# Kernel tuning notes

Hardware: AMD Instinct MI355X
Metric: run time of the kernel (lower is better)

Reference implementation:

```python
import jax, jax.numpy as jnp
import numpy as np

K = 10
NUM_BLKS = 6
LN_EPS = 1e-6
NODE_D = 64


def layer_norm(x, g, b):
    m = jnp.mean(x, axis=-1, keepdims=True)
    v = jnp.var(x, axis=-1, keepdims=True)
    return (x - m) * jax.lax.rsqrt(v + LN_EPS) * g + b


def setup_inputs() -> dict:
    key = jax.random.key(0)
    B, N_c, N_t, D_S, D_F = 4, 4096, 1024, 3, 4
    D_IN = 4 + D_S + D_F  # obs-embed(4) + s + f
    ks = jax.random.split(key, 32)
    sc = 0.02
    inp = {
        "s_ctx": jax.random.normal(ks[0], (B, N_c, D_S), jnp.float32),
        "f_ctx": jax.random.normal(ks[1], (B, N_c, D_F), jnp.float32),
        "s_test": jax.random.normal(ks[2], (B, N_t, D_S), jnp.float32),
        "valid_lens_ctx": jax.random.randint(ks[3], (B,), N_c // 2, N_c + 1).astype(jnp.int32),
        # embed_obs: nn.Embed(2, 4)
        "emb_obs": jax.random.normal(ks[4], (2, 4), jnp.float32) * sc,
        # embed_all: MLP([256,128,64], gelu)
        "ea_W0": jax.random.normal(ks[5], (D_IN, 256), jnp.float32) * sc, "ea_b0": jnp.zeros((256,), jnp.float32),
        "ea_W1": jax.random.normal(ks[6], (256, 128), jnp.float32) * sc, "ea_b1": jnp.zeros((128,), jnp.float32),
        "ea_W2": jax.random.normal(ks[7], (128, NODE_D), jnp.float32) * sc, "ea_b2": jnp.zeros((NODE_D,), jnp.float32),
        # top-level LayerNorm
        "ln_g": jnp.ones((NODE_D,), jnp.float32), "ln_b": jnp.zeros((NODE_D,), jnp.float32),
        # GraphKRBlock params, stacked over NUM_BLKS blocks
        "blk_Wm0": jax.random.normal(ks[8], (NUM_BLKS, NODE_D + 1, 128), jnp.float32) * sc,
        "blk_bm0": jnp.zeros((NUM_BLKS, 128), jnp.float32),
        "blk_Wm1": jax.random.normal(ks[9], (NUM_BLKS, 128, NODE_D), jnp.float32) * sc,
        "blk_bm1": jnp.zeros((NUM_BLKS, NODE_D), jnp.float32),
        "blk_Wu0": jax.random.normal(ks[10], (NUM_BLKS, 2 * NODE_D, 128), jnp.float32) * sc,
        "blk_bu0": jnp.zeros((NUM_BLKS, 128), jnp.float32),
        "blk_Wu1": jax.random.normal(ks[11], (NUM_BLKS, 128, NODE_D), jnp.float32) * sc,
        "blk_bu1": jnp.zeros((NUM_BLKS, NODE_D), jnp.float32),
        "blk_lng": jnp.ones((NUM_BLKS, NODE_D), jnp.float32),
        "blk_lnb": jnp.zeros((NUM_BLKS, NODE_D), jnp.float32),
        # head: MLP([256,64,2], gelu)
        "hd_W0": jax.random.normal(ks[12], (NODE_D, 256), jnp.float32) * sc, "hd_b0": jnp.zeros((256,), jnp.float32),
        "hd_W1": jax.random.normal(ks[13], (256, 64), jnp.float32) * sc, "hd_b1": jnp.zeros((64,), jnp.float32),
        "hd_W2": jax.random.normal(ks[14], (64, 2), jnp.float32) * sc, "hd_b2": jnp.zeros((2,), jnp.float32),
    }
    return inp


def reference(s_ctx, f_ctx, s_test, valid_lens_ctx,
              emb_obs, ea_W0, ea_b0, ea_W1, ea_b1, ea_W2, ea_b2, ln_g, ln_b,
              blk_Wm0, blk_bm0, blk_Wm1, blk_bm1, blk_Wu0, blk_bu0, blk_Wu1, blk_bu1,
              blk_lng, blk_lnb, hd_W0, hd_b0, hd_W1, hd_b1, hd_W2, hd_b2):
    B, N_c, _ = s_ctx.shape
    N_t = s_test.shape[1]

    # --- per-sample O(n^2) KNN graph build (custom_k_nearest_senders, l2 dist) ---
    mask = jnp.arange(N_c)[None, :] < valid_lens_ctx[:, None]          # [B,N_c]
    s_send = jnp.where(mask[..., None], s_ctx, 1e6)                    # invalid -> far away
    rx = jnp.concatenate([s_ctx, s_test], axis=1)                      # [B,N,d_s] receivers
    d = jnp.sqrt(jnp.sum((rx[:, :, None, :] - s_send[:, None, :, :]) ** 2, axis=-1))  # [B,N,N_c]
    negd, senders = jax.lax.top_k(-d, K)                               # k-nearest: [B,N,K]
    dists = -negd                                                       # ascending distances

    # --- embeddings: stack(embed_obs, s, f) -> embed_all MLP -> LayerNorm ---
    def embed(x):
        h = jax.nn.gelu(x @ ea_W0 + ea_b0)
        h = jax.nn.gelu(h @ ea_W1 + ea_b1)
        h = h @ ea_W2 + ea_b2
        return layer_norm(h, ln_g, ln_b)

    ctx_in = jnp.concatenate(
        [jnp.broadcast_to(emb_obs[1], (B, N_c, emb_obs.shape[1])), s_ctx, f_ctx], axis=-1)
    test_in = jnp.concatenate(
        [jnp.broadcast_to(emb_obs[0], (B, N_t, emb_obs.shape[1])), s_test,
         jnp.zeros((B, N_t, f_ctx.shape[-1]), f_ctx.dtype)], axis=-1)
    nodes = jnp.concatenate([embed(ctx_in), embed(test_in)], axis=1)   # [B,N,64]

    # --- num_blks GraphKRBlock message-passing blocks ---
    bidx = jnp.arange(B)[:, None, None]
    w = jax.nn.softmax(-dists, axis=-1)                                # kernel weights per receiver
    for i in range(NUM_BLKS):
        sf = nodes[bidx, senders]                                      # gather senders [B,N,K,64]
        m_in = jnp.concatenate([sf, dists[..., None]], axis=-1)        # [B,N,K,65]
        m = jax.nn.gelu(m_in @ blk_Wm0[i] + blk_bm0[i]) @ blk_Wm1[i] + blk_bm1[i]
        agg = jnp.einsum('bnk,bnkd->bnd', w, m)                        # scatter-to-receivers
        u_in = jnp.concatenate([nodes, agg], axis=-1)                  # [B,N,128]
        upd = jax.nn.gelu(u_in @ blk_Wu0[i] + blk_bu0[i]) @ blk_Wu1[i] + blk_bu1[i]
        nodes = layer_norm(nodes + upd, blk_lng[i], blk_lnb[i])

    # --- head on test nodes ---
    x_t = nodes[:, N_c:, :]                                            # [B,N_t,64]
    h = jax.nn.gelu(x_t @ hd_W0 + hd_b0)
    h = jax.nn.gelu(h @ hd_W1 + hd_b1)
    f_dist = h @ hd_W2 + hd_b2                                         # [B,N_t,2]
    f_mu, f_log_var = jnp.split(f_dist, 2, axis=-1)
    f_std = jnp.exp(f_log_var / 2)                                     # min_std = 0.0
    return f_mu, f_std
```

## Files before the change

kernel.cpp:

```cpp
#include <hip/hip_runtime.h>
#include <math.h>

#define BB 4
#define NC 4096
#define NT 1024
#define NN (NC + NT)
#define NODES (BB * NN)
#define DD 64
#define KNN 10
#define NBLK 6
#define BIGF 3.0e38f
#define LM 5

typedef __attribute__((ext_vector_type(8))) short short8;
typedef __attribute__((ext_vector_type(4))) float f32x4;
typedef __attribute__((ext_vector_type(4))) int int4v;

__device__ __forceinline__ unsigned short f2bf(float f) {
    unsigned int u = __float_as_uint(f);
    unsigned int r = (u + 0x7fffu + ((u >> 16) & 1u)) >> 16;
    return (unsigned short)r;
}
__device__ __forceinline__ float bf2f(unsigned short h) {
    return __uint_as_float(((unsigned int)h) << 16);
}

__device__ __forceinline__ float gelu_f(float x) {
    const float c0 = 0.7978845608028654f;
    float x3 = x * x * x;
    float z2 = 2.0f * c0 * (x + 0.044715f * x3);
    float e = __expf(z2);
    float r = __builtin_amdgcn_rcpf(1.0f + e);
    return x - x * r;
}

__device__ __forceinline__ float wave_sum(float v) {
#pragma unroll
    for (int off = 32; off > 0; off >>= 1) v += __shfl_xor(v, off, 64);
    return v;
}

__device__ __forceinline__ f32x4 mfma_bf16(short8 a, short8 b, f32x4 c) {
    asm("v_mfma_f32_16x16x32_bf16 %0, %1, %2, %0" : "+v"(c) : "v"(a), "v"(b));
    return c;
}


__global__ __launch_bounds__(256) void k_convw(
    const float* __restrict__ Wm0, const float* __restrict__ Wm1,
    const float* __restrict__ Wu0, const float* __restrict__ Wu1,
    const float* __restrict__ bm0,
    const float* __restrict__ eW0, const float* __restrict__ eW1,
    const float* __restrict__ eW2,
    const float* __restrict__ hW0, const float* __restrict__ hW1,
    const float* __restrict__ sctx, const int* __restrict__ valid_lens,
    unsigned short* __restrict__ wtm0, unsigned short* __restrict__ wtm1p,
    unsigned short* __restrict__ wtu0, unsigned short* __restrict__ wtu1,
    float* __restrict__ wdp, float* __restrict__ bm0p,
    unsigned short* __restrict__ wte0, unsigned short* __restrict__ wte1,
    unsigned short* __restrict__ wte2,
    unsigned short* __restrict__ wth0, unsigned short* __restrict__ wth1,
    float4* __restrict__ s4)
{
    int t = blockIdx.x * 256 + threadIdx.x;
    if (t < 49152) {
        int i = t / 8192, r = t % 8192, n = r / 64, k = r % 64;
        wtm0[t] = f2bf(Wm0[(i * 65 + k) * 128 + n]);
    } else if (t < 98304) {
        int u = t - 49152;
        int i = u / 8192, r = u % 8192, n = r / 128, cp = r % 128;
        int col = ((cp & 7) << 4) | (cp >> 3);
        wtm1p[u] = f2bf(Wm1[(i * 128 + col) * 64 + n]);
    } else if (t < 196608) {
        int u = t - 98304;
        int i = u / 16384, r = u % 16384, n = r / 128, k = r % 128;
        wtu0[u] = f2bf(Wu0[(i * 128 + k) * 128 + n]);
    } else if (t < 245760) {
        int u = t - 196608;
        int i = u / 8192, r = u % 8192, n = r / 128, k = r % 128;
        wtu1[u] = f2bf(Wu1[(i * 128 + k) * 64 + n]);
    } else if (t < 246528) {
        int u = t - 245760;
        int i = u / 128, cp = u % 128;
        int col = ((cp & 7) << 4) | (cp >> 3);
        wdp[u] = Wm0[(i * 65 + 64) * 128 + col];
    } else if (t < 247296) {
        int u = t - 246528;
        int i = u / 128, cp = u % 128;
        int col = ((cp & 7) << 4) | (cp >> 3);
        bm0p[u] = bm0[i * 128 + col];
    } else if (t < 255488) {
        int u = t - 247296;
        int n = u / 32, k = u % 32;
        wte0[u] = (k < 11) ? f2bf(eW0[k * 256 + n]) : 0;
    } else if (t < 288256) {
        int u = t - 255488;
        int n = u / 256, k = u % 256;
        wte1[u] = f2bf(eW1[k * 128 + n]);
    } else if (t < 296448) {
        int u = t - 288256;
        int n = u / 128, k = u % 128;
        wte2[u] = f2bf(eW2[k * 64 + n]);
    } else if (t < 312832) {
        int u = t - 296448;
        int n = u / 64, k = u % 64;
        wth0[u] = f2bf(hW0[k * 256 + n]);
    } else if (t < 329216) {
        int u = t - 312832;
        int n = u / 256, k = u % 256;
        wth1[u] = f2bf(hW1[k * 64 + n]);
    } else if (t < 329216 + BB * NC) {
        int u = t - 329216;
        int b = u / NC, j = u % NC;
        bool ok = j < valid_lens[b];
        float x = ok ? sctx[u * 3] : 1.0e6f;
        float y = ok ? sctx[u * 3 + 1] : 1.0e6f;
        float z = ok ? sctx[u * 3 + 2] : 1.0e6f;
        s4[u] = make_float4(x, y, z, 0.0f);
    }
}

__global__ __launch_bounds__(256) void k_embed2(
    const float* __restrict__ s_ctx, const float* __restrict__ f_ctx,
    const float* __restrict__ s_test, const float* __restrict__ emb_obs,
    const unsigned short* __restrict__ WT0, const float* __restrict__ b0,
    const unsigned short* __restrict__ WT1, const float* __restrict__ b1,
    const unsigned short* __restrict__ WT2, const float* __restrict__ b2,
    const float* __restrict__ g, const float* __restrict__ bta,
    const unsigned short* __restrict__ Wm0n,
    unsigned short* __restrict__ nodes,
    unsigned short* __restrict__ Pout)
{
    __shared__ unsigned short H0[4][16 * 256];
    __shared__ unsigned short H1[4][16 * 128];
    __shared__ unsigned short XO[4][16 * 64];
    int t = threadIdx.x;
    int wave = t >> 6, lane = t & 63, lr = lane & 15, lk = lane >> 4;
    int rb = wave * 16;
    int n0 = blockIdx.x * 64;
    int bq = n0 / NN, nloc0 = n0 % NN;
    bool is_ctx = nloc0 < NC;
    int nr = nloc0 + rb + lr;
    float xv[8];
#pragma unroll
    for (int j = 0; j < 8; ++j) xv[j] = 0.0f;
    if (lk == 0) {
        const float* eb = emb_obs + (is_ctx ? 4 : 0);
        xv[0] = eb[0]; xv[1] = eb[1]; xv[2] = eb[2]; xv[3] = eb[3];
        if (is_ctx) {
            const float* sp = s_ctx + ((size_t)(bq * NC + nr)) * 3;
            const float* fp = f_ctx + ((size_t)(bq * NC + nr)) * 4;
            xv[4] = sp[0]; xv[5] = sp[1]; xv[6] = sp[2]; xv[7] = fp[0];
        } else {
            const float* sp = s_test + ((size_t)(bq * NT + nr - NC)) * 3;
            xv[4] = sp[0]; xv[5] = sp[1]; xv[6] = sp[2];
        }
    } else if (lk == 1 && is_ctx) {
        const float* fp = f_ctx + ((size_t)(bq * NC + nr)) * 4;
        xv[0] = fp[1]; xv[1] = fp[2]; xv[2] = fp[3];
    }
    short8 a;
#pragma unroll
    for (int j = 0; j < 8; ++j) a[j] = (short)f2bf(xv[j]);

    f32x4 acc0[16];
#pragma unroll
    for (int nt = 0; nt < 16; ++nt) {
        short8 bb = *(const short8*)(WT0 + (nt * 16 + lr) * 32 + lk * 8);
        f32x4 z = (f32x4){0.f, 0.f, 0.f, 0.f};
        acc0[nt] = mfma_bf16(a, bb, z);
    }
    unsigned short* h0 = &H0[wave][0];
#pragma unroll
    for (int nt = 0; nt < 16; ++nt) {
        int col = nt * 16 + lr;
        float bias = b0[col];
        int u = col >> 3;
#pragma unroll
        for (int j = 0; j < 4; ++j) {
            int row = lk * 4 + j;
            float v = gelu_f(acc0[nt][j] + bias);
            int us = (u & 16) | ((u ^ row) & 15);
            h0[row * 256 + us * 8 + (col & 7)] = f2bf(v);
        }
    }
    f32x4 acc1[8];
#pragma unroll
    for (int nt = 0; nt < 8; ++nt) acc1[nt] = (f32x4){0.f, 0.f, 0.f, 0.f};
#pragma unroll
    for (int ks = 0; ks < 8; ++ks) {
        int u = ks * 4 + lk;
        int us = (u & 16) | ((u ^ lr) & 15);
        short8 aa = *(const short8*)(&h0[lr * 256 + us * 8]);
#pragma unroll
        for (int nt = 0; nt < 8; ++nt) {
            short8 bb = *(const short8*)(WT1 + (nt * 16 + lr) * 256 + ks * 32 + lk * 8);
            acc1[nt] = mfma_bf16(aa, bb, acc1[nt]);
        }
    }
    unsigned short* h1 = &H1[wave][0];
#pragma unroll
    for (int nt = 0; nt < 8; ++nt) {
        int col = nt * 16 + lr;
        float bias = b1[col];
        int u = col >> 3;
#pragma unroll
        for (int j = 0; j < 4; ++j) {
            int row = lk * 4 + j;
            float v = gelu_f(acc1[nt][j] + bias);
            int us = (u ^ row) & 15;
            h1[row * 128 + us * 8 + (col & 7)] = f2bf(v);
        }
    }
    f32x4 acc2[4];
#pragma unroll
    for (int nt = 0; nt < 4; ++nt) acc2[nt] = (f32x4){0.f, 0.f, 0.f, 0.f};
#pragma unroll
    for (int ks = 0; ks < 4; ++ks) {
        int u = ks * 4 + lk;
        int us = (u ^ lr) & 15;
        short8 aa = *(const short8*)(&h1[lr * 128 + us * 8]);
#pragma unroll
        for (int nt = 0; nt < 4; ++nt) {
            short8 bb = *(const short8*)(WT2 + (nt * 16 + lr) * 128 + ks * 32 + lk * 8);
            acc2[nt] = mfma_bf16(aa, bb, acc2[nt]);
        }
    }
    float vals[4][4];
#pragma unroll
    for (int j = 0; j < 4; ++j)
#pragma unroll
        for (int nt = 0; nt < 4; ++nt)
            vals[j][nt] = acc2[nt][j] + b2[nt * 16 + lr];
    unsigned short* xo = &XO[wave][0];
#pragma unroll
    for (int j = 0; j < 4; ++j) {
        float s = vals[j][0] + vals[j][1] + vals[j][2] + vals[j][3];
#pragma unroll
        for (int m = 1; m < 16; m <<= 1) s += __shfl_xor(s, m, 64);
        float mean = s * (1.0f / 64.0f);
        float vs = 0.0f;
#pragma unroll
        for (int nt = 0; nt < 4; ++nt) { float d = vals[j][nt] - mean; vs += d * d; }
#pragma unroll
        for (int m = 1; m < 16; m <<= 1) vs += __shfl_xor(vs, m, 64);
        float inv = rsqrtf(vs * (1.0f / 64.0f) + 1e-6f);
        int row = lk * 4 + j;
        int node = n0 + rb + row;
#pragma unroll
        for (int nt = 0; nt < 4; ++nt) {
            int col = nt * 16 + lr;
            float o = (vals[j][nt] - mean) * inv * g[col] + bta[col];
            unsigned short ob = f2bf(o);
            nodes[(size_t)node * 64 + col] = ob;
            xo[row * 64 + ((col >> 3) ^ (row & 7)) * 8 + (col & 7)] = ob;
        }
    }
    f32x4 accP[8];
#pragma unroll
    for (int nt = 0; nt < 8; ++nt) accP[nt] = (f32x4){0.f, 0.f, 0.f, 0.f};
#pragma unroll
    for (int ks = 0; ks < 2; ++ks) {
        short8 aa = *(const short8*)(&xo[lr * 64 + ((ks * 4 + lk) ^ (lr & 7)) * 8]);
#pragma unroll
        for (int nt = 0; nt < 8; ++nt) {
            short8 bb = *(const short8*)(Wm0n + (nt * 16 + lr) * 64 + ks * 32 + lk * 8);
            accP[nt] = mfma_bf16(aa, bb, accP[nt]);
        }
    }
#pragma unroll
    for (int j = 0; j < 4; ++j) {
        int node = n0 + rb + lk * 4 + j;
        short8 ps;
#pragma unroll
        for (int nt = 0; nt < 8; ++nt) ps[nt] = (short)f2bf(accP[nt][j]);
        *(short8*)(Pout + (size_t)node * 128 + lr * 8) = ps;
    }
}

__global__ __launch_bounds__(256) void k_topk(
    const float4* __restrict__ s4, const float* __restrict__ s_ctx,
    const float* __restrict__ s_test,
    float* __restrict__ dists, int* __restrict__ senders, float* __restrict__ wout)
{
    __shared__ float cd[4 * 64 * 11];
    __shared__ float slotv[4][4][16];
    __shared__ int   sloti[4][4][16];
    __shared__ int   cnt[4][4];
    int wave = threadIdx.x >> 6;
    int lane = threadIdx.x & 63;
    int r0 = blockIdx.x * 16 + wave * 4;
    int b = r0 / NN;
    const float4* sc = s4 + (size_t)b * NC;
    float px[4], py[4], pz[4];
#pragma unroll
    for (int q = 0; q < 4; ++q) {
        int n = (r0 + q) % NN;
        const float* p = (n < NC) ? &s_ctx[(size_t)(b * NC + n) * 3]
                                  : &s_test[(size_t)(b * NT + (n - NC)) * 3];
        px[q] = p[0]; py[q] = p[1]; pz[q] = p[2];
    }
    float bq[4][LM];
#pragma unroll
    for (int q = 0; q < 4; ++q)
#pragma unroll
        for (int k = 0; k < LM; ++k) bq[q][k] = BIGF;
#pragma unroll 8
    for (int i = 0; i < 64; ++i) {
        int j = lane + (i << 6);
        float4 s = sc[j];
#pragma unroll
        for (int q = 0; q < 4; ++q) {
            float dx = px[q] - s.x, dy = py[q] - s.y, dz = pz[q] - s.z;
            float d2 = fmaf(dx, dx, fmaf(dy, dy, dz * dz));
#pragma unroll
            for (int k = LM - 1; k >= 1; --k)
                bq[q][k] = __builtin_amdgcn_fmed3f(bq[q][k - 1], bq[q][k], d2);
            bq[q][0] = fminf(bq[q][0], d2);
        }
    }
    int base = (wave * 64 + lane) * 11;
    float T[4];
#pragma unroll
    for (int q = 0; q < 4; ++q) {
#pragma unroll
        for (int k = 0; k < LM; ++k) cd[base + k] = bq[q][k];
        cd[base + LM] = BIGF;
        __builtin_amdgcn_wave_barrier();
        int head = 0;
        float Tl = BIGF;
#pragma unroll
        for (int rr = 0; rr < KNN; ++rr) {
            float v = cd[base + head];
            float mv = v;
#pragma unroll
            for (int off = 32; off > 0; off >>= 1) mv = fminf(mv, __shfl_xor(mv, off, 64));
            unsigned long long ball = __ballot(v == mv);
            int win = __ffsll(ball) - 1;
            if (lane == win) head++;
            Tl = mv;
        }
        T[q] = Tl;
    }
    if (lane < 4) cnt[wave][lane] = 0;
    __builtin_amdgcn_wave_barrier();
#pragma unroll 4
    for (int i = 0; i < 64; ++i) {
        int j = lane + (i << 6);
        float4 s = sc[j];
#pragma unroll
        for (int q = 0; q < 4; ++q) {
            float dx = px[q] - s.x, dy = py[q] - s.y, dz = pz[q] - s.z;
            float v = fmaf(dx, dx, fmaf(dy, dy, dz * dz));
            if (v <= T[q]) {
                int slot = atomicAdd(&cnt[wave][q], 1);
                if (slot < 16) { slotv[wave][q][slot] = v; sloti[wave][q][slot] = j; }
            }
        }
    }
    __builtin_amdgcn_wave_barrier();
#pragma unroll
    for (int q = 0; q < 4; ++q) {
        int count = cnt[wave][q];
        if (count > 16) count = 16;
        float e = 0.0f, d = 0.0f;
        int isel = 0, rank = 0;
        bool own = lane < count;
        if (own) {
            float myv = slotv[wave][q][lane];
            int myi = sloti[wave][q][lane];
            for (int j = 0; j < count; ++j) {
                float vj = slotv[wave][q][j];
                int ij = sloti[wave][q][j];
                rank += (vj < myv || (vj == myv && ij < myi)) ? 1 : 0;
            }
            own = rank < KNN;
            if (own) {
                isel = myi;
                d = sqrtf(myv);
                e = __expf(-d);
            }
        }
        float ssum = wave_sum(e);
        if (own) {
            size_t o = (size_t)(r0 + q) * KNN + rank;
            dists[o] = d;
            senders[o] = isel;
            wout[o] = e / ssum;
        }
    }
}

__global__ __launch_bounds__(256) void k_blk(
    const unsigned short* __restrict__ nodes_in,
    const unsigned short* __restrict__ P,
    const float* __restrict__ dists, const int* __restrict__ senders,
    const float* __restrict__ w,
    const float* __restrict__ wdp, const float* __restrict__ bm0p,
    const unsigned short* __restrict__ Wm1p,
    const float* __restrict__ bm1,
    const unsigned short* __restrict__ WTu0,
    const float* __restrict__ bu0,
    const unsigned short* __restrict__ WTu1,
    const float* __restrict__ bu1,
    const float* __restrict__ lng, const float* __restrict__ lnb,
    const unsigned short* __restrict__ Wm0n,
    const int doP,
    unsigned short* __restrict__ nodes_out,
    unsigned short* __restrict__ Pout,
    const int doHead, const int testOnly,
    const unsigned short* __restrict__ wth0,
    const float* __restrict__ hb0,
    const unsigned short* __restrict__ wth1,
    const float* __restrict__ hb1,
    const float* __restrict__ hW2, const float* __restrict__ hb2,
    float* __restrict__ out)
{
    __shared__ unsigned short X[16 * 64];
    __shared__ unsigned short G[16 * 128];
    __shared__ unsigned short AG[16 * 64];
    __shared__ unsigned short H[16 * 128];
    __shared__ unsigned short XO[16 * 64];
    __shared__ unsigned short HH[16 * 256];
    __shared__ unsigned short HH1[16 * 72];
    __shared__ int   sidE[160];
    __shared__ float dE[160], wE[160];
    int l = threadIdx.x;
    int wave = l >> 6, lane = l & 63;
    int bid = blockIdx.x;
    int tile = testOnly ? ((bid >> 6) * 320 + 256 + (bid & 63))
                        : ((bid & 7) * 160 + (bid >> 3));
    int n0 = tile * 16;
    int b = n0 / NN;
    size_t bbase = (size_t)b * NN;
    int e0 = n0 * KNN;
    if (l < 160) {
        sidE[l] = senders[e0 + l];
        dE[l]   = dists[e0 + l];
        wE[l]   = w[e0 + l];
    }
    if (l < 128) {
        int row = l >> 3, u = l & 7;
        int4v v = *(const int4v*)(nodes_in + ((size_t)(n0 + row)) * 64 + u * 8);
        *(int4v*)(&X[row * 64 + (u ^ (row & 7)) * 8]) = v;
    }
    __syncthreads();
    float wd0 = wdp[2 * lane], wd1 = wdp[2 * lane + 1];
    float bb0 = bm0p[2 * lane], bb1 = bm0p[2 * lane + 1];
    const unsigned int* Pb = (const unsigned int*)P;
    unsigned int* G32 = (unsigned int*)G;
#pragma unroll
    for (int nn = 0; nn < 4; ++nn) {
        int n = wave * 4 + nn;
        float a0 = 0.0f, a1 = 0.0f;
#pragma unroll
        for (int k = 0; k < KNN; ++k) {
            int e = n * KNN + k;
            int sid = sidE[e];
            float dd = dE[e], ww = wE[e];
            unsigned int pr = Pb[(bbase + sid) * 64 + lane];
            float p0 = __uint_as_float(pr << 16);
            float p1 = __uint_as_float(pr & 0xFFFF0000u);
            float g0 = gelu_f(fmaf(dd, wd0, p0 + bb0));
            float g1 = gelu_f(fmaf(dd, wd1, p1 + bb1));
            a0 = fmaf(ww, g0, a0);
            a1 = fmaf(ww, g1, a1);
        }
        unsigned int pk = (unsigned int)f2bf(a0) | ((unsigned int)f2bf(a1) << 16);
        G32[n * 64 + ((lane >> 2) ^ n) * 4 + (lane & 3)] = pk;
    }
    __syncthreads();
    if (wave != 0) return;
    int lr = lane & 15, lk = lane >> 4;
    f32x4 accA[4];
#pragma unroll
    for (int nt = 0; nt < 4; ++nt) accA[nt] = (f32x4){0.f, 0.f, 0.f, 0.f};
#pragma unroll
    for (int ks = 0; ks < 4; ++ks) {
        short8 a = *(const short8*)(&G[lr * 128 + ((ks * 4 + lk) ^ lr) * 8]);
#pragma unroll
        for (int nt = 0; nt < 4; ++nt) {
            short8 bb = *(const short8*)(Wm1p + (nt * 16 + lr) * 128 + ks * 32 + lk * 8);
            accA[nt] = mfma_bf16(a, bb, accA[nt]);
        }
    }
#pragma unroll
    for (int nt = 0; nt < 4; ++nt) {
        int col = nt * 16 + lr;
        float bias = bm1[col];
#pragma unroll
        for (int j = 0; j < 4; ++j) {
            int row = lk * 4 + j;
            AG[row * 64 + ((col >> 3) ^ (row & 7)) * 8 + (col & 7)] =
                f2bf(accA[nt][j] + bias);
        }
    }
    f32x4 acc[8];
#pragma unroll
    for (int nt = 0; nt < 8; ++nt) acc[nt] = (f32x4){0.f, 0.f, 0.f, 0.f};
#pragma unroll
    for (int ks = 0; ks < 4; ++ks) {
        short8 a;
        if (ks < 2) a = *(const short8*)(&X[lr * 64 + ((ks * 4 + lk) ^ (lr & 7)) * 8]);
        else        a = *(const short8*)(&AG[lr * 64 + (((ks - 2) * 4 + lk) ^ (lr & 7)) * 8]);
#pragma unroll
        for (int nt = 0; nt < 8; ++nt) {
            short8 bb = *(const short8*)(WTu0 + (nt * 16 + lr) * 128 + ks * 32 + lk * 8);
            acc[nt] = mfma_bf16(a, bb, acc[nt]);
        }
    }
#pragma unroll
    for (int nt = 0; nt < 8; ++nt) {
        int col = nt * 16 + lr;
        float bias = bu0[col];
#pragma unroll
        for (int j = 0; j < 4; ++j) {
            int lrow = lk * 4 + j;
            float v = gelu_f(acc[nt][j] + bias);
            H[lrow * 128 + ((col >> 3) ^ lrow) * 8 + (col & 7)] = f2bf(v);
        }
    }
    f32x4 acc2[4];
#pragma unroll
    for (int nt = 0; nt < 4; ++nt) acc2[nt] = (f32x4){0.f, 0.f, 0.f, 0.f};
#pragma unroll
    for (int ks = 0; ks < 4; ++ks) {
        short8 a = *(const short8*)(&H[lr * 128 + ((ks * 4 + lk) ^ lr) * 8]);
#pragma unroll
        for (int nt = 0; nt < 4; ++nt) {
            short8 bb = *(const short8*)(WTu1 + (nt * 16 + lr) * 128 + ks * 32 + lk * 8);
            acc2[nt] = mfma_bf16(a, bb, acc2[nt]);
        }
    }
    float vals[4][4];
#pragma unroll
    for (int j = 0; j < 4; ++j) {
        int row = lk * 4 + j;
#pragma unroll
        for (int nt = 0; nt < 4; ++nt) {
            int col = nt * 16 + lr;
            float x = bf2f(X[row * 64 + ((col >> 3) ^ (row & 7)) * 8 + (col & 7)]);
            vals[j][nt] = x + acc2[nt][j] + bu1[col];
        }
    }
#pragma unroll
    for (int j = 0; j < 4; ++j) {
        int row = lk * 4 + j;
        float s = vals[j][0] + vals[j][1] + vals[j][2] + vals[j][3];
#pragma unroll
        for (int mm = 1; mm < 16; mm <<= 1) s += __shfl_xor(s, mm, 64);
        float mean = s * (1.0f / 64.0f);
        float vs = 0.0f;
#pragma unroll
        for (int nt = 0; nt < 4; ++nt) { float d = vals[j][nt] - mean; vs += d * d; }
#pragma unroll
        for (int mm = 1; mm < 16; mm <<= 1) vs += __shfl_xor(vs, mm, 64);
        float inv = rsqrtf(vs * (1.0f / 64.0f) + 1e-6f);
#pragma unroll
        for (int nt = 0; nt < 4; ++nt) {
            int col = nt * 16 + lr;
            float o = (vals[j][nt] - mean) * inv * lng[col] + lnb[col];
            unsigned short ob = f2bf(o);
            nodes_out[((size_t)(n0 + row)) * 64 + col] = ob;
            XO[row * 64 + ((col >> 3) ^ (row & 7)) * 8 + (col & 7)] = ob;
        }
    }
    if (doP) {
        f32x4 accP[8];
#pragma unroll
        for (int nt = 0; nt < 8; ++nt) accP[nt] = (f32x4){0.f, 0.f, 0.f, 0.f};
#pragma unroll
        for (int ks = 0; ks < 2; ++ks) {
            short8 aa = *(const short8*)(&XO[lr * 64 + ((ks * 4 + lk) ^ (lr & 7)) * 8]);
#pragma unroll
            for (int nt = 0; nt < 8; ++nt) {
                short8 bb = *(const short8*)(Wm0n + (nt * 16 + lr) * 64 + ks * 32 + lk * 8);
                accP[nt] = mfma_bf16(aa, bb, accP[nt]);
            }
        }
#pragma unroll
        for (int j = 0; j < 4; ++j) {
            int node = n0 + lk * 4 + j;
            short8 ps;
#pragma unroll
            for (int nt = 0; nt < 8; ++nt) ps[nt] = (short)f2bf(accP[nt][j]);
            *(short8*)(Pout + (size_t)node * 128 + lr * 8) = ps;
        }
    }
    if (doHead) {
        int nloc = n0 % NN;
        int bq = n0 / NN;
#pragma unroll
        for (int half = 0; half < 2; ++half) {
            f32x4 ah[8];
#pragma unroll
            for (int nt = 0; nt < 8; ++nt) ah[nt] = (f32x4){0.f, 0.f, 0.f, 0.f};
#pragma unroll
            for (int ks = 0; ks < 2; ++ks) {
                short8 aa = *(const short8*)(&XO[lr * 64 + ((ks * 4 + lk) ^ (lr & 7)) * 8]);
#pragma unroll
                for (int nt = 0; nt < 8; ++nt) {
                    int col16 = half * 8 + nt;
                    short8 bb = *(const short8*)(wth0 + (col16 * 16 + lr) * 64 + ks * 32 + lk * 8);
                    ah[nt] = mfma_bf16(aa, bb, ah[nt]);
                }
            }
#pragma unroll
            for (int nt = 0; nt < 8; ++nt) {
                int col = (half * 8 + nt) * 16 + lr;
                float bias = hb0[col];
                int u = col >> 3;
#pragma unroll
                for (int j = 0; j < 4; ++j) {
                    int row = lk * 4 + j;
                    float v = gelu_f(ah[nt][j] + bias);
                    int us = (u & 16) | ((u ^ row) & 15);
                    HH[row * 256 + us * 8 + (col & 7)] = f2bf(v);
                }
            }
        }
        f32x4 a1h[4];
#pragma unroll
        for (int nt = 0; nt < 4; ++nt) a1h[nt] = (f32x4){0.f, 0.f, 0.f, 0.f};
#pragma unroll
        for (int ks = 0; ks < 8; ++ks) {
            int u = ks * 4 + lk;
            int us = (u & 16) | ((u ^ lr) & 15);
            short8 aa = *(const short8*)(&HH[lr * 256 + us * 8]);
#pragma unroll
            for (int nt = 0; nt < 4; ++nt) {
                short8 bb = *(const short8*)(wth1 + (nt * 16 + lr) * 256 + ks * 32 + lk * 8);
                a1h[nt] = mfma_bf16(aa, bb, a1h[nt]);
            }
        }
#pragma unroll
        for (int nt = 0; nt < 4; ++nt) {
            int col = nt * 16 + lr;
            float bias = hb1[col];
#pragma unroll
            for (int j = 0; j < 4; ++j) {
                int row = lk * 4 + j;
                HH1[row * 72 + col] = f2bf(gelu_f(a1h[nt][j] + bias));
            }
        }
        int task = lane >> 1;
        int row = task >> 1;
        int o = task & 1;
        int t2 = lane & 1;
        float pp = 0.0f;
#pragma unroll
        for (int d = 0; d < 32; ++d) {
            int dd = t2 * 32 + d;
            pp += bf2f(HH1[row * 72 + dd]) * hW2[dd * 2 + o];
        }
        pp += __shfl_xor(pp, 1, 64);
        if (t2 == 0) {
            int gg = bq * NT + (nloc - NC) + row;
            if (o == 0) out[gg] = pp + hb2[0];
            else        out[BB * NT + gg] = __expf(0.5f * (pp + hb2[1]));
        }
    }
}

extern "C" void kernel_launch(void* const* d_in, const int* in_sizes, int n_in,
                              void* d_out, int out_size, void* d_ws, size_t ws_size,
                              hipStream_t stream)
{
    (void)in_sizes; (void)n_in; (void)out_size; (void)ws_size;
    const float* s_ctx   = (const float*)d_in[0];
    const float* f_ctx   = (const float*)d_in[1];
    const float* s_test  = (const float*)d_in[2];
    const int*   valid   = (const int*)d_in[3];
    const float* emb_obs = (const float*)d_in[4];
    const float* ea_W0   = (const float*)d_in[5];
    const float* ea_b0   = (const float*)d_in[6];
    const float* ea_W1   = (const float*)d_in[7];
    const float* ea_b1   = (const float*)d_in[8];
    const float* ea_W2   = (const float*)d_in[9];
    const float* ea_b2   = (const float*)d_in[10];
    const float* ln_g    = (const float*)d_in[11];
    const float* ln_b    = (const float*)d_in[12];
    const float* blk_Wm0 = (const float*)d_in[13];
    const float* blk_bm0 = (const float*)d_in[14];
    const float* blk_Wm1 = (const float*)d_in[15];
    const float* blk_bm1 = (const float*)d_in[16];
    const float* blk_Wu0 = (const float*)d_in[17];
    const float* blk_bu0 = (const float*)d_in[18];
    const float* blk_Wu1 = (const float*)d_in[19];
    const float* blk_bu1 = (const float*)d_in[20];
    const float* blk_lng = (const float*)d_in[21];
    const float* blk_lnb = (const float*)d_in[22];
    const float* hd_W0   = (const float*)d_in[23];
    const float* hd_b0   = (const float*)d_in[24];
    const float* hd_W1   = (const float*)d_in[25];
    const float* hd_b1   = (const float*)d_in[26];
    const float* hd_W2   = (const float*)d_in[27];
    const float* hd_b2   = (const float*)d_in[28];

    char* p = (char*)d_ws;
    auto alloc = [&](size_t bytes) { char* r = p; p += (bytes + 255) & ~(size_t)255; return r; };
    unsigned short* nodesA = (unsigned short*)alloc((size_t)NODES * 64 * 2);
    unsigned short* nodesB = (unsigned short*)alloc((size_t)NODES * 64 * 2);
    unsigned short* PA     = (unsigned short*)alloc((size_t)NODES * 128 * 2);
    unsigned short* PB     = (unsigned short*)alloc((size_t)NODES * 128 * 2);
    float* dists   = (float*)alloc((size_t)NODES * KNN * 4);
    float* wbuf    = (float*)alloc((size_t)NODES * KNN * 4);
    int*   senders = (int*)alloc((size_t)NODES * KNN * 4);
    unsigned short* wtm0  = (unsigned short*)alloc((size_t)6 * 8192 * 2);
    unsigned short* wtm1p = (unsigned short*)alloc((size_t)6 * 8192 * 2);
    unsigned short* wtu0  = (unsigned short*)alloc((size_t)6 * 16384 * 2);
    unsigned short* wtu1  = (unsigned short*)alloc((size_t)6 * 8192 * 2);
    float* wdp  = (float*)alloc((size_t)6 * 128 * 4);
    float* bm0p = (float*)alloc((size_t)6 * 128 * 4);
    unsigned short* wte0 = (unsigned short*)alloc((size_t)8192 * 2);
    unsigned short* wte1 = (unsigned short*)alloc((size_t)32768 * 2);
    unsigned short* wte2 = (unsigned short*)alloc((size_t)8192 * 2);
    unsigned short* wth0 = (unsigned short*)alloc((size_t)16384 * 2);
    unsigned short* wth1 = (unsigned short*)alloc((size_t)16384 * 2);
    float4* s4 = (float4*)alloc((size_t)BB * NC * 16);

    k_convw<<<1350, 256, 0, stream>>>(
        blk_Wm0, blk_Wm1, blk_Wu0, blk_Wu1, blk_bm0,
        ea_W0, ea_W1, ea_W2, hd_W0, hd_W1, s_ctx, valid,
        wtm0, wtm1p, wtu0, wtu1, wdp, bm0p, wte0, wte1, wte2, wth0, wth1, s4);

    k_embed2<<<NODES / 64, 256, 0, stream>>>(s_ctx, f_ctx, s_test, emb_obs,
        wte0, ea_b0, wte1, ea_b1, wte2, ea_b2, ln_g, ln_b, wtm0, nodesA, PA);

    k_topk<<<NODES / 16, 256, 0, stream>>>(s4, s_ctx, s_test,
                                           dists, senders, wbuf);

    unsigned short* nin = nodesA; unsigned short* nout = nodesB;
    unsigned short* pin = PA;     unsigned short* pout = PB;
    for (int i = 0; i < NBLK; ++i) {
        int doP = (i < NBLK - 1) ? 1 : 0;
        int doHead = (i == NBLK - 1) ? 1 : 0;
        int testOnly = doHead;
        int grid = testOnly ? (BB * NT / 16) : (NODES / 16);
        const unsigned short* wm0n = wtm0 + (size_t)((i + 1) % NBLK) * 8192;
        k_blk<<<grid, 256, 0, stream>>>(nin, pin, dists, senders, wbuf,
            wdp + (size_t)i * 128, bm0p + (size_t)i * 128,
            wtm1p + (size_t)i * 8192, blk_bm1 + (size_t)i * 64,
            wtu0 + (size_t)i * 16384, blk_bu0 + (size_t)i * 128,
            wtu1 + (size_t)i * 8192, blk_bu1 + (size_t)i * 64,
            blk_lng + (size_t)i * 64, blk_lnb + (size_t)i * 64,
            wm0n, doP, nout, pout,
            doHead, testOnly, wth0, hd_b0, wth1, hd_b1, hd_W2, hd_b2, (float*)d_out);
        unsigned short* tmp = nin; nin = nout; nout = tmp;
        tmp = pin; pin = pout; pout = tmp;
    }
}
```

Before: 287.6 us.

## Fuse embedding MLP into top-k kernel tail, one wave per block

```diff
diff --git a/kernel.cpp b/kernel.cpp
--- a/kernel.cpp
+++ b/kernel.cpp
@@ -120,173 +120,26 @@
     }
 }
 
-__global__ __launch_bounds__(256) void k_embed2(
-    const float* __restrict__ s_ctx, const float* __restrict__ f_ctx,
-    const float* __restrict__ s_test, const float* __restrict__ emb_obs,
+__global__ __launch_bounds__(256) void k_topk(
+    const float4* __restrict__ s4, const float* __restrict__ s_ctx,
+    const float* __restrict__ s_test, const float* __restrict__ f_ctx,
+    const float* __restrict__ emb_obs,
     const unsigned short* __restrict__ WT0, const float* __restrict__ b0,
     const unsigned short* __restrict__ WT1, const float* __restrict__ b1,
     const unsigned short* __restrict__ WT2, const float* __restrict__ b2,
     const float* __restrict__ g, const float* __restrict__ bta,
     const unsigned short* __restrict__ Wm0n,
     unsigned short* __restrict__ nodes,
-    unsigned short* __restrict__ Pout)
-{
-    __shared__ unsigned short H0[4][16 * 256];
-    __shared__ unsigned short H1[4][16 * 128];
-    __shared__ unsigned short XO[4][16 * 64];
-    int t = threadIdx.x;
-    int wave = t >> 6, lane = t & 63, lr = lane & 15, lk = lane >> 4;
-    int rb = wave * 16;
-    int n0 = blockIdx.x * 64;
-    int bq = n0 / NN, nloc0 = n0 % NN;
-    bool is_ctx = nloc0 < NC;
-    int nr = nloc0 + rb + lr;
-    float xv[8];
-#pragma unroll
-    for (int j = 0; j < 8; ++j) xv[j] = 0.0f;
-    if (lk == 0) {
-        const float* eb = emb_obs + (is_ctx ? 4 : 0);
-        xv[0] = eb[0]; xv[1] = eb[1]; xv[2] = eb[2]; xv[3] = eb[3];
-        if (is_ctx) {
-            const float* sp = s_ctx + ((size_t)(bq * NC + nr)) * 3;
-            const float* fp = f_ctx + ((size_t)(bq * NC + nr)) * 4;
-            xv[4] = sp[0]; xv[5] = sp[1]; xv[6] = sp[2]; xv[7] = fp[0];
-        } else {
-            const float* sp = s_test + ((size_t)(bq * NT + nr - NC)) * 3;
-            xv[4] = sp[0]; xv[5] = sp[1]; xv[6] = sp[2];
-        }
-    } else if (lk == 1 && is_ctx) {
-        const float* fp = f_ctx + ((size_t)(bq * NC + nr)) * 4;
-        xv[0] = fp[1]; xv[1] = fp[2]; xv[2] = fp[3];
-    }
-    short8 a;
-#pragma unroll
-    for (int j = 0; j < 8; ++j) a[j] = (short)f2bf(xv[j]);
-
-    f32x4 acc0[16];
-#pragma unroll
-    for (int nt = 0; nt < 16; ++nt) {
-        short8 bb = *(const short8*)(WT0 + (nt * 16 + lr) * 32 + lk * 8);
-        f32x4 z = (f32x4){0.f, 0.f, 0.f, 0.f};
-        acc0[nt] = mfma_bf16(a, bb, z);
-    }
-    unsigned short* h0 = &H0[wave][0];
-#pragma unroll
-    for (int nt = 0; nt < 16; ++nt) {
-        int col = nt * 16 + lr;
-        float bias = b0[col];
-        int u = col >> 3;
-#pragma unroll
-        for (int j = 0; j < 4; ++j) {
-            int row = lk * 4 + j;
-            float v = gelu_f(acc0[nt][j] + bias);
-            int us = (u & 16) | ((u ^ row) & 15);
-            h0[row * 256 + us * 8 + (col & 7)] = f2bf(v);
-        }
-    }
-    f32x4 acc1[8];
-#pragma unroll
-    for (int nt = 0; nt < 8; ++nt) acc1[nt] = (f32x4){0.f, 0.f, 0.f, 0.f};
-#pragma unroll
-    for (int ks = 0; ks < 8; ++ks) {
-        int u = ks * 4 + lk;
-        int us = (u & 16) | ((u ^ lr) & 15);
-        short8 aa = *(const short8*)(&h0[lr * 256 + us * 8]);
-#pragma unroll
-        for (int nt = 0; nt < 8; ++nt) {
-            short8 bb = *(const short8*)(WT1 + (nt * 16 + lr) * 256 + ks * 32 + lk * 8);
-            acc1[nt] = mfma_bf16(aa, bb, acc1[nt]);
-        }
-    }
-    unsigned short* h1 = &H1[wave][0];
-#pragma unroll
-    for (int nt = 0; nt < 8; ++nt) {
-        int col = nt * 16 + lr;
-        float bias = b1[col];
-        int u = col >> 3;
-#pragma unroll
-        for (int j = 0; j < 4; ++j) {
-            int row = lk * 4 + j;
-            float v = gelu_f(acc1[nt][j] + bias);
-            int us = (u ^ row) & 15;
-            h1[row * 128 + us * 8 + (col & 7)] = f2bf(v);
-        }
-    }
-    f32x4 acc2[4];
-#pragma unroll
-    for (int nt = 0; nt < 4; ++nt) acc2[nt] = (f32x4){0.f, 0.f, 0.f, 0.f};
-#pragma unroll
-    for (int ks = 0; ks < 4; ++ks) {
-        int u = ks * 4 + lk;
-        int us = (u ^ lr) & 15;
-        short8 aa = *(const short8*)(&h1[lr * 128 + us * 8]);
-#pragma unroll
-        for (int nt = 0; nt < 4; ++nt) {
-            short8 bb = *(const short8*)(WT2 + (nt * 16 + lr) * 128 + ks * 32 + lk * 8);
-            acc2[nt] = mfma_bf16(aa, bb, acc2[nt]);
-        }
-    }
-    float vals[4][4];
-#pragma unroll
-    for (int j = 0; j < 4; ++j)
-#pragma unroll
-        for (int nt = 0; nt < 4; ++nt)
-            vals[j][nt] = acc2[nt][j] + b2[nt * 16 + lr];
-    unsigned short* xo = &XO[wave][0];
-#pragma unroll
-    for (int j = 0; j < 4; ++j) {
-        float s = vals[j][0] + vals[j][1] + vals[j][2] + vals[j][3];
-#pragma unroll
-        for (int m = 1; m < 16; m <<= 1) s += __shfl_xor(s, m, 64);
-        float mean = s * (1.0f / 64.0f);
-        float vs = 0.0f;
-#pragma unroll
-        for (int nt = 0; nt < 4; ++nt) { float d = vals[j][nt] - mean; vs += d * d; }
-#pragma unroll
-        for (int m = 1; m < 16; m <<= 1) vs += __shfl_xor(vs, m, 64);
-        float inv = rsqrtf(vs * (1.0f / 64.0f) + 1e-6f);
-        int row = lk * 4 + j;
-        int node = n0 + rb + row;
-#pragma unroll
-        for (int nt = 0; nt < 4; ++nt) {
-            int col = nt * 16 + lr;
-            float o = (vals[j][nt] - mean) * inv * g[col] + bta[col];
-            unsigned short ob = f2bf(o);
-            nodes[(size_t)node * 64 + col] = ob;
-            xo[row * 64 + ((col >> 3) ^ (row & 7)) * 8 + (col & 7)] = ob;
-        }
-    }
-    f32x4 accP[8];
-#pragma unroll
-    for (int nt = 0; nt < 8; ++nt) accP[nt] = (f32x4){0.f, 0.f, 0.f, 0.f};
-#pragma unroll
-    for (int ks = 0; ks < 2; ++ks) {
-        short8 aa = *(const short8*)(&xo[lr * 64 + ((ks * 4 + lk) ^ (lr & 7)) * 8]);
-#pragma unroll
-        for (int nt = 0; nt < 8; ++nt) {
-            short8 bb = *(const short8*)(Wm0n + (nt * 16 + lr) * 64 + ks * 32 + lk * 8);
-            accP[nt] = mfma_bf16(aa, bb, accP[nt]);
-        }
-    }
-#pragma unroll
-    for (int j = 0; j < 4; ++j) {
-        int node = n0 + rb + lk * 4 + j;
-        short8 ps;
-#pragma unroll
-        for (int nt = 0; nt < 8; ++nt) ps[nt] = (short)f2bf(accP[nt][j]);
-        *(short8*)(Pout + (size_t)node * 128 + lr * 8) = ps;
-    }
-}
-
-__global__ __launch_bounds__(256) void k_topk(
-    const float4* __restrict__ s4, const float* __restrict__ s_ctx,
-    const float* __restrict__ s_test,
+    unsigned short* __restrict__ Pout,
     float* __restrict__ dists, int* __restrict__ senders, float* __restrict__ wout)
 {
     __shared__ float cd[4 * 64 * 11];
     __shared__ float slotv[4][4][16];
     __shared__ int   sloti[4][4][16];
     __shared__ int   cnt[4][4];
+    __shared__ unsigned short h0s[16 * 256];
+    __shared__ unsigned short h1s[16 * 128];
+    __shared__ unsigned short xos[16 * 64];
     int wave = threadIdx.x >> 6;
     int lane = threadIdx.x & 63;
     int r0 = blockIdx.x * 16 + wave * 4;
@@ -387,6 +240,159 @@
             dists[o] = d;
             senders[o] = isel;
             wout[o] = e / ssum;
+        }
+    }
+    if (wave != 0) return;
+
+    {
+        int lr = lane & 15, lk = lane >> 4;
+        int n0 = blockIdx.x * 16;
+        int bq2 = n0 / NN, nloc0 = n0 % NN;
+        bool is_ctx = nloc0 < NC;
+        int nr = nloc0 + lr;
+        float xv[8];
+#pragma unroll
+        for (int j = 0; j < 8; ++j) xv[j] = 0.0f;
+        if (lk == 0) {
+            const float* eb = emb_obs + (is_ctx ? 4 : 0);
+            xv[0] = eb[0]; xv[1] = eb[1]; xv[2] = eb[2]; xv[3] = eb[3];
+            if (is_ctx) {
+                const float* sp = s_ctx + ((size_t)(bq2 * NC + nr)) * 3;
+                const float* fp = f_ctx + ((size_t)(bq2 * NC + nr)) * 4;
+                xv[4] = sp[0]; xv[5] = sp[1]; xv[6] = sp[2]; xv[7] = fp[0];
+            } else {
+                const float* sp = s_test + ((size_t)(bq2 * NT + nr - NC)) * 3;
+                xv[4] = sp[0]; xv[5] = sp[1]; xv[6] = sp[2];
+            }
+        } else if (lk == 1 && is_ctx) {
+            const float* fp = f_ctx + ((size_t)(bq2 * NC + nr)) * 4;
+            xv[0] = fp[1]; xv[1] = fp[2]; xv[2] = fp[3];
+        }
+        short8 a;
+#pragma unroll
+        for (int j = 0; j < 8; ++j) a[j] = (short)f2bf(xv[j]);
+
+#pragma unroll
+        for (int gq = 0; gq < 4; ++gq) {
+            f32x4 acc0[4];
+#pragma unroll
+            for (int n4 = 0; n4 < 4; ++n4) {
+                int nt = gq * 4 + n4;
+                short8 bb = *(const short8*)(WT0 + (nt * 16 + lr) * 32 + lk * 8);
+                f32x4 z = (f32x4){0.f, 0.f, 0.f, 0.f};
+                acc0[n4] = mfma_bf16(a, bb, z);
+            }
+#pragma unroll
+            for (int n4 = 0; n4 < 4; ++n4) {
+                int col = (gq * 4 + n4) * 16 + lr;
+                float bias = b0[col];
+                int u = col >> 3;
+#pragma unroll
+                for (int j = 0; j < 4; ++j) {
+                    int row = lk * 4 + j;
+                    float v = gelu_f(acc0[n4][j] + bias);
+                    int us = (u & 16) | ((u ^ row) & 15);
+                    h0s[row * 256 + us * 8 + (col & 7)] = f2bf(v);
+                }
+            }
+        }
+#pragma unroll
+        for (int half = 0; half < 2; ++half) {
+            f32x4 acc1[4];
+#pragma unroll
+            for (int n4 = 0; n4 < 4; ++n4) acc1[n4] = (f32x4){0.f, 0.f, 0.f, 0.f};
+#pragma unroll
+            for (int ks = 0; ks < 8; ++ks) {
+                int u = ks * 4 + lk;
+                int us = (u & 16) | ((u ^ lr) & 15);
+                short8 aa = *(const short8*)(&h0s[lr * 256 + us * 8]);
+#pragma unroll
+                for (int n4 = 0; n4 < 4; ++n4) {
+                    int nt = half * 4 + n4;
+                    short8 bb = *(const short8*)(WT1 + (nt * 16 + lr) * 256 + ks * 32 + lk * 8);
+                    acc1[n4] = mfma_bf16(aa, bb, acc1[n4]);
+                }
+            }
+#pragma unroll
+            for (int n4 = 0; n4 < 4; ++n4) {
+                int col = (half * 4 + n4) * 16 + lr;
+                float bias = b1[col];
+                int u = col >> 3;
+#pragma unroll
+                for (int j = 0; j < 4; ++j) {
+                    int row = lk * 4 + j;
+                    float v = gelu_f(acc1[n4][j] + bias);
+                    int us = (u ^ row) & 15;
+                    h1s[row * 128 + us * 8 + (col & 7)] = f2bf(v);
+                }
+            }
+        }
+        f32x4 acc2[4];
+#pragma unroll
+        for (int nt = 0; nt < 4; ++nt) acc2[nt] = (f32x4){0.f, 0.f, 0.f, 0.f};
+#pragma unroll
+        for (int ks = 0; ks < 4; ++ks) {
+            int u = ks * 4 + lk;
+            int us = (u ^ lr) & 15;
+            short8 aa = *(const short8*)(&h1s[lr * 128 + us * 8]);
+#pragma unroll
+            for (int nt = 0; nt < 4; ++nt) {
+                short8 bb = *(const short8*)(WT2 + (nt * 16 + lr) * 128 + ks * 32 + lk * 8);
+                acc2[nt] = mfma_bf16(aa, bb, acc2[nt]);
+            }
+        }
+        float vals[4][4];
+#pragma unroll
+        for (int j = 0; j < 4; ++j)
+#pragma unroll
+            for (int nt = 0; nt < 4; ++nt)
+                vals[j][nt] = acc2[nt][j] + b2[nt * 16 + lr];
+#pragma unroll
+        for (int j = 0; j < 4; ++j) {
+            int row = lk * 4 + j;
+            float s = vals[j][0] + vals[j][1] + vals[j][2] + vals[j][3];
+#pragma unroll
+            for (int m = 1; m < 16; m <<= 1) s += __shfl_xor(s, m, 64);
+            float mean = s * (1.0f / 64.0f);
+            float vs = 0.0f;
+#pragma unroll
+            for (int nt = 0; nt < 4; ++nt) { float dd = vals[j][nt] - mean; vs += dd * dd; }
+#pragma unroll
+            for (int m = 1; m < 16; m <<= 1) vs += __shfl_xor(vs, m, 64);
+            float inv = rsqrtf(vs * (1.0f / 64.0f) + 1e-6f);
+            int node = n0 + row;
+#pragma unroll
+            for (int nt = 0; nt < 4; ++nt) {
+                int col = nt * 16 + lr;
+                float o = (vals[j][nt] - mean) * inv * g[col] + bta[col];
+                unsigned short ob = f2bf(o);
+                nodes[(size_t)node * 64 + col] = ob;
+                xos[row * 64 + ((col >> 3) ^ (row & 7)) * 8 + (col & 7)] = ob;
+            }
+        }
+#pragma unroll
+        for (int half = 0; half < 2; ++half) {
+            f32x4 accP[4];
+#pragma unroll
+            for (int n4 = 0; n4 < 4; ++n4) accP[n4] = (f32x4){0.f, 0.f, 0.f, 0.f};
+#pragma unroll
+            for (int ks = 0; ks < 2; ++ks) {
+                short8 aa = *(const short8*)(&xos[lr * 64 + ((ks * 4 + lk) ^ (lr & 7)) * 8]);
+#pragma unroll
+                for (int n4 = 0; n4 < 4; ++n4) {
+                    int nt = half * 4 + n4;
+                    short8 bb = *(const short8*)(Wm0n + (nt * 16 + lr) * 64 + ks * 32 + lk * 8);
+                    accP[n4] = mfma_bf16(aa, bb, accP[n4]);
+                }
+            }
+#pragma unroll
+            for (int j = 0; j < 4; ++j) {
+                int node = n0 + lk * 4 + j;
+                uint2 pk2;
+                pk2.x = (unsigned int)f2bf(accP[0][j]) | ((unsigned int)f2bf(accP[1][j]) << 16);
+                pk2.y = (unsigned int)f2bf(accP[2][j]) | ((unsigned int)f2bf(accP[3][j]) << 16);
+                *(uint2*)(Pout + (size_t)node * 128 + lr * 8 + half * 4) = pk2;
+            }
         }
     }
 }
@@ -724,11 +730,9 @@
         ea_W0, ea_W1, ea_W2, hd_W0, hd_W1, s_ctx, valid,
         wtm0, wtm1p, wtu0, wtu1, wdp, bm0p, wte0, wte1, wte2, wth0, wth1, s4);
 
-    k_embed2<<<NODES / 64, 256, 0, stream>>>(s_ctx, f_ctx, s_test, emb_obs,
-        wte0, ea_b0, wte1, ea_b1, wte2, ea_b2, ln_g, ln_b, wtm0, nodesA, PA);
-
-    k_topk<<<NODES / 16, 256, 0, stream>>>(s4, s_ctx, s_test,
-                                           dists, senders, wbuf);
+    k_topk<<<NODES / 16, 256, 0, stream>>>(s4, s_ctx, s_test, f_ctx, emb_obs,
+        wte0, ea_b0, wte1, ea_b1, wte2, ea_b2, ln_g, ln_b, wtm0,
+        nodesA, PA, dists, senders, wbuf);
 
     unsigned short* nin = nodesA; unsigned short* nout = nodesB;
     unsigned short* pin = PA;     unsigned short* pout = PB;
```

After: 308.1 us. 1.07x slower.

## Split per-tile MLP matmuls across two waves with LDS handoff

Applied to the files above, without the earlier changes.

```diff
diff --git a/kernel.cpp b/kernel.cpp
--- a/kernel.cpp
+++ b/kernel.cpp
@@ -421,6 +421,7 @@
     __shared__ unsigned short AG[16 * 64];
     __shared__ unsigned short H[16 * 128];
     __shared__ unsigned short XO[16 * 64];
+    __shared__ float VF[16 * 65];
     __shared__ unsigned short HH[16 * 256];
     __shared__ unsigned short HH1[16 * 72];
     __shared__ int   sidE[160];
@@ -470,102 +471,124 @@
         G32[n * 64 + ((lane >> 2) ^ n) * 4 + (lane & 3)] = pk;
     }
     __syncthreads();
-    if (wave != 0) return;
     int lr = lane & 15, lk = lane >> 4;
-    f32x4 accA[4];
-#pragma unroll
-    for (int nt = 0; nt < 4; ++nt) accA[nt] = (f32x4){0.f, 0.f, 0.f, 0.f};
-#pragma unroll
-    for (int ks = 0; ks < 4; ++ks) {
-        short8 a = *(const short8*)(&G[lr * 128 + ((ks * 4 + lk) ^ lr) * 8]);
-#pragma unroll
-        for (int nt = 0; nt < 4; ++nt) {
-            short8 bb = *(const short8*)(Wm1p + (nt * 16 + lr) * 128 + ks * 32 + lk * 8);
-            accA[nt] = mfma_bf16(a, bb, accA[nt]);
-        }
-    }
-#pragma unroll
-    for (int nt = 0; nt < 4; ++nt) {
-        int col = nt * 16 + lr;
-        float bias = bm1[col];
+    if (wave < 2) {
+        f32x4 accA[2];
+#pragma unroll
+        for (int n2 = 0; n2 < 2; ++n2) accA[n2] = (f32x4){0.f, 0.f, 0.f, 0.f};
+#pragma unroll
+        for (int ks = 0; ks < 4; ++ks) {
+            short8 a = *(const short8*)(&G[lr * 128 + ((ks * 4 + lk) ^ lr) * 8]);
+#pragma unroll
+            for (int n2 = 0; n2 < 2; ++n2) {
+                int nt = wave * 2 + n2;
+                short8 bb = *(const short8*)(Wm1p + (nt * 16 + lr) * 128 + ks * 32 + lk * 8);
+                accA[n2] = mfma_bf16(a, bb, accA[n2]);
+            }
+        }
+#pragma unroll
+        for (int n2 = 0; n2 < 2; ++n2) {
+            int col = (wave * 2 + n2) * 16 + lr;
+            float bias = bm1[col];
+#pragma unroll
+            for (int j = 0; j < 4; ++j) {
+                int row = lk * 4 + j;
+                AG[row * 64 + ((col >> 3) ^ (row & 7)) * 8 + (col & 7)] =
+                    f2bf(accA[n2][j] + bias);
+            }
+        }
+    }
+    __syncthreads();
+    if (wave < 2) {
+        f32x4 acc[4];
+#pragma unroll
+        for (int n4 = 0; n4 < 4; ++n4) acc[n4] = (f32x4){0.f, 0.f, 0.f, 0.f};
+#pragma unroll
+        for (int ks = 0; ks < 4; ++ks) {
+            short8 a;
+            if (ks < 2) a = *(const short8*)(&X[lr * 64 + ((ks * 4 + lk) ^ (lr & 7)) * 8]);
+            else        a = *(const short8*)(&AG[lr * 64 + (((ks - 2) * 4 + lk) ^ (lr & 7)) * 8]);
+#pragma unroll
+            for (int n4 = 0; n4 < 4; ++n4) {
+                int nt = wave * 4 + n4;
+                short8 bb = *(const short8*)(WTu0 + (nt * 16 + lr) * 128 + ks * 32 + lk * 8);
+                acc[n4] = mfma_bf16(a, bb, acc[n4]);
+            }
+        }
+#pragma unroll
+        for (int n4 = 0; n4 < 4; ++n4) {
+            int col = (wave * 4 + n4) * 16 + lr;
+            float bias = bu0[col];
+#pragma unroll
+            for (int j = 0; j < 4; ++j) {
+                int lrow = lk * 4 + j;
+                float v = gelu_f(acc[n4][j] + bias);
+                H[lrow * 128 + ((col >> 3) ^ lrow) * 8 + (col & 7)] = f2bf(v);
+            }
+        }
+    }
+    __syncthreads();
+    if (wave < 2) {
+        f32x4 acc2[2];
+#pragma unroll
+        for (int n2 = 0; n2 < 2; ++n2) acc2[n2] = (f32x4){0.f, 0.f, 0.f, 0.f};
+#pragma unroll
+        for (int ks = 0; ks < 4; ++ks) {
+            short8 a = *(const short8*)(&H[lr * 128 + ((ks * 4 + lk) ^ lr) * 8]);
+#pragma unroll
+            for (int n2 = 0; n2 < 2; ++n2) {
+                int nt = wave * 2 + n2;
+                short8 bb = *(const short8*)(WTu1 + (nt * 16 + lr) * 128 + ks * 32 + lk * 8);
+                acc2[n2] = mfma_bf16(a, bb, acc2[n2]);
+            }
+        }
+#pragma unroll
+        for (int n2 = 0; n2 < 2; ++n2) {
+            int col = (wave * 2 + n2) * 16 + lr;
+            float bias = bu1[col];
+#pragma unroll
+            for (int j = 0; j < 4; ++j) {
+                int row = lk * 4 + j;
+                float x = bf2f(X[row * 64 + ((col >> 3) ^ (row & 7)) * 8 + (col & 7)]);
+                VF[row * 65 + col] = x + acc2[n2][j] + bias;
+            }
+        }
+    }
+    __syncthreads();
+    if (wave == 0) {
+        float vals[4][4];
 #pragma unroll
         for (int j = 0; j < 4; ++j) {
             int row = lk * 4 + j;
-            AG[row * 64 + ((col >> 3) ^ (row & 7)) * 8 + (col & 7)] =
-                f2bf(accA[nt][j] + bias);
-        }
-    }
-    f32x4 acc[8];
-#pragma unroll
-    for (int nt = 0; nt < 8; ++nt) acc[nt] = (f32x4){0.f, 0.f, 0.f, 0.f};
-#pragma unroll
-    for (int ks = 0; ks < 4; ++ks) {
-        short8 a;
-        if (ks < 2) a = *(const short8*)(&X[lr * 64 + ((ks * 4 + lk) ^ (lr & 7)) * 8]);
-        else        a = *(const short8*)(&AG[lr * 64 + (((ks - 2) * 4 + lk) ^ (lr & 7)) * 8]);
-#pragma unroll
-        for (int nt = 0; nt < 8; ++nt) {
-            short8 bb = *(const short8*)(WTu0 + (nt * 16 + lr) * 128 + ks * 32 + lk * 8);
-            acc[nt] = mfma_bf16(a, bb, acc[nt]);
-        }
-    }
-#pragma unroll
-    for (int nt = 0; nt < 8; ++nt) {
-        int col = nt * 16 + lr;
-        float bias = bu0[col];
+#pragma unroll
+            for (int nt = 0; nt < 4; ++nt)
+                vals[j][nt] = VF[row * 65 + nt * 16 + lr];
+        }
 #pragma unroll
         for (int j = 0; j < 4; ++j) {
-            int lrow = lk * 4 + j;
-            float v = gelu_f(acc[nt][j] + bias);
-            H[lrow * 128 + ((col >> 3) ^ lrow) * 8 + (col & 7)] = f2bf(v);
-        }
-    }
-    f32x4 acc2[4];
-#pragma unroll
-    for (int nt = 0; nt < 4; ++nt) acc2[nt] = (f32x4){0.f, 0.f, 0.f, 0.f};
-#pragma unroll
-    for (int ks = 0; ks < 4; ++ks) {
-        short8 a = *(const short8*)(&H[lr * 128 + ((ks * 4 + lk) ^ lr) * 8]);
-#pragma unroll
-        for (int nt = 0; nt < 4; ++nt) {
-            short8 bb = *(const short8*)(WTu1 + (nt * 16 + lr) * 128 + ks * 32 + lk * 8);
-            acc2[nt] = mfma_bf16(a, bb, acc2[nt]);
-        }
-    }
-    float vals[4][4];
-#pragma unroll
-    for (int j = 0; j < 4; ++j) {
-        int row = lk * 4 + j;
-#pragma unroll
-        for (int nt = 0; nt < 4; ++nt) {
-            int col = nt * 16 + lr;
-            float x = bf2f(X[row * 64 + ((col >> 3) ^ (row & 7)) * 8 + (col & 7)]);
-            vals[j][nt] = x + acc2[nt][j] + bu1[col];
-        }
-    }
-#pragma unroll
-    for (int j = 0; j < 4; ++j) {
-        int row = lk * 4 + j;
-        float s = vals[j][0] + vals[j][1] + vals[j][2] + vals[j][3];
-#pragma unroll
-        for (int mm = 1; mm < 16; mm <<= 1) s += __shfl_xor(s, mm, 64);
-        float mean = s * (1.0f / 64.0f);
-        float vs = 0.0f;
-#pragma unroll
-        for (int nt = 0; nt < 4; ++nt) { float d = vals[j][nt] - mean; vs += d * d; }
-#pragma unroll
-        for (int mm = 1; mm < 16; mm <<= 1) vs += __shfl_xor(vs, mm, 64);
-        float inv = rsqrtf(vs * (1.0f / 64.0f) + 1e-6f);
-#pragma unroll
-        for (int nt = 0; nt < 4; ++nt) {
-            int col = nt * 16 + lr;
-            float o = (vals[j][nt] - mean) * inv * lng[col] + lnb[col];
-            unsigned short ob = f2bf(o);
-            nodes_out[((size_t)(n0 + row)) * 64 + col] = ob;
-            XO[row * 64 + ((col >> 3) ^ (row & 7)) * 8 + (col & 7)] = ob;
-        }
-    }
-    if (doP) {
+            int row = lk * 4 + j;
+            float s = vals[j][0] + vals[j][1] + vals[j][2] + vals[j][3];
+#pragma unroll
+            for (int mm = 1; mm < 16; mm <<= 1) s += __shfl_xor(s, mm, 64);
+            float mean = s * (1.0f / 64.0f);
+            float vs = 0.0f;
+#pragma unroll
+            for (int nt = 0; nt < 4; ++nt) { float d = vals[j][nt] - mean; vs += d * d; }
+#pragma unroll
+            for (int mm = 1; mm < 16; mm <<= 1) vs += __shfl_xor(vs, mm, 64);
+            float inv = rsqrtf(vs * (1.0f / 64.0f) + 1e-6f);
+#pragma unroll
+            for (int nt = 0; nt < 4; ++nt) {
+                int col = nt * 16 + lr;
+                float o = (vals[j][nt] - mean) * inv * lng[col] + lnb[col];
+                unsigned short ob = f2bf(o);
+                nodes_out[((size_t)(n0 + row)) * 64 + col] = ob;
+                XO[row * 64 + ((col >> 3) ^ (row & 7)) * 8 + (col & 7)] = ob;
+            }
+        }
+    }
+    __syncthreads();
+    if (doP && wave == 1) {
         f32x4 accP[8];
 #pragma unroll
         for (int nt = 0; nt < 8; ++nt) accP[nt] = (f32x4){0.f, 0.f, 0.f, 0.f};
@@ -587,7 +610,7 @@
             *(short8*)(Pout + (size_t)node * 128 + lr * 8) = ps;
         }
     }
-    if (doHead) {
+    if (doHead && wave == 0) {
         int nloc = n0 % NN;
         int bq = n0 / NN;
 #pragma unroll
```

Result: faster. 267.5 us (-7.0%).
